# Performance work log

Hardware: AMD Instinct MI355X
Metric: run time of the kernel (lower is better)

The kernel has to match this reference:

```python
import jax, jax.numpy as jnp
import numpy as np

VERY_NEG = -1e11
VERY_SMALL = 1e-10
PAGERANK_LAMBDA = 0.8
FACT_SCALE = 3.0


def _linear(x, W, b):
    return x @ W.T + b


def _lstm(x, Wih, Whh, bih, bhh):
    # single-layer unidirectional LSTM, pytorch gate order (i, f, g, o)
    B, T, _ = x.shape
    H = Whh.shape[1]
    def step(carry, xt):
        h, c = carry
        g = xt @ Wih.T + bih + h @ Whh.T + bhh
        i, f, gg, o = jnp.split(g, 4, axis=-1)
        c = jax.nn.sigmoid(f) * c + jax.nn.sigmoid(i) * jnp.tanh(gg)
        h = jax.nn.sigmoid(o) * jnp.tanh(c)
        return (h, c), h
    init = (jnp.zeros((B, H), x.dtype), jnp.zeros((B, H), x.dtype))
    (h_last, _), hs = jax.lax.scan(step, init, jnp.swapaxes(x, 0, 1))
    return jnp.swapaxes(hs, 0, 1), h_last


def _forward(local_entity, q2e_adj_mat, kb_fact_rel, query_text, e2f_entity, f2e_entity,
             answer_dist, word_emb, entity_emb, rel_emb, ent_W, ent_b, rel_W, rel_b,
             lstm_Wih, lstm_Whh, lstm_bih, lstm_bhh, q2e_W, q2e_b, head_W, head_b,
             tail_W, tail_b, self_W, self_b, e2e_W, e2e_b, score_W, score_b):
    B, E = local_entity.shape
    D = ent_W.shape[0]
    num_word = word_emb.shape[0] - 1
    num_entity = entity_emb.shape[0] - 1
    b_idx = jnp.arange(B)[:, None]  # (B,1) for batched gather/scatter

    # --- query LSTM encoder ---
    query_mask = (query_text != num_word).astype(jnp.float32)            # (B,Q)
    qh, q_last = _lstm(word_emb[query_text], lstm_Wih, lstm_Whh, lstm_bih, lstm_bhh)
    query_node_emb = q_last[:, None, :]                                   # (B,1,D)

    # --- fact embeddings + fact-query attention weights ---
    local_fact_emb = _linear(rel_emb[kb_fact_rel], rel_W, rel_b)          # (B,F,D)
    div = jnp.sqrt(jnp.asarray(D, jnp.float32))
    sim = jnp.einsum('bqd,bfd->bqf', qh, local_fact_emb) / div
    sim = jax.nn.softmax(sim + (1.0 - query_mask)[:, :, None] * VERY_NEG, axis=1)
    att = jnp.einsum('bqf,bqd->bfd', sim, qh)                             # (B,F,D)
    Wf = jnp.sum(att * local_fact_emb, axis=2) / div                      # (B,F)
    W_tilde = jnp.exp(Wf - jnp.max(Wf, axis=1, keepdims=True))
    # e2f_softmax[b,e] = sum of W_tilde over facts whose head is e (sparse e2f^T @ W_tilde)
    e2f_softmax = jnp.maximum(
        jnp.zeros((B, E), jnp.float32).at[b_idx, e2f_entity].add(W_tilde), VERY_SMALL)

    # --- entity embeddings (word_dim != entity_dim -> entity_linear) ---
    local_entity_emb = _linear(entity_emb[local_entity], ent_W, ent_b)    # (B,E,D)
    pagerank_f = q2e_adj_mat[:, :, 0]                                     # (B,E)

    n_layer = q2e_W.shape[0]
    for i in range(n_layer):
        q2e_emb = jnp.broadcast_to(_linear(query_node_emb, q2e_W[i], q2e_b[i]), (B, E, D))
        # entity -> fact: gather head-entity messages
        head = _linear(local_entity_emb, head_W[i], head_b[i])            # (B,E,D)
        e2f_emb = jax.nn.relu(
            _linear(local_fact_emb, self_W[i], self_b[i]) + head[b_idx, e2f_entity])
        pr = pagerank_f / e2f_softmax                                     # (B,E)
        e2f_norm = (W_tilde * pr[b_idx, e2f_entity])[:, :, None]          # (B,F,1)
        e2f_emb = e2f_emb * e2f_norm
        # fact -> entity: scatter-add to tail entities
        tail = _linear(e2f_emb, tail_W[i], tail_b[i])                     # (B,F,D)
        f2e_emb = jax.nn.relu(
            _linear(local_entity_emb, self_W[i], self_b[i])
            + jnp.zeros((B, E, D), jnp.float32).at[b_idx, f2e_entity].add(tail))
        pagerank_f = (PAGERANK_LAMBDA
                      * jnp.zeros((B, E), jnp.float32).at[b_idx, f2e_entity].add(e2f_norm[:, :, 0])
                      + (1.0 - PAGERANK_LAMBDA) * pagerank_f)
        nxt = jnp.concatenate([local_entity_emb, q2e_emb, FACT_SCALE * f2e_emb], axis=2)
        local_entity_emb = jax.nn.relu(_linear(nxt, e2e_W[i], e2e_b[i]))

    score = local_entity_emb @ score_W + score_b                          # (B,E)
    mask = (local_entity != num_entity).astype(jnp.float32)
    score = score + (1.0 - mask) * VERY_NEG
    return jax.nn.sigmoid(score) * mask


def setup_inputs() -> dict:
    key = jax.random.key(0)
    ks = jax.random.split(key, 24)
    B, E, Fc, Q = 8, 2000, 12000, 20
    WD, D = 300, 100
    NE, NW, NR, L = 100000, 40000, 300, 3
    f32 = jnp.float32
    def nrm(k, shape, scale):
        return jax.random.normal(k, shape, f32) * scale
    return {
        'local_entity': jax.random.randint(ks[0], (B, E), 0, NE),
        'q2e_adj_mat': jax.random.uniform(ks[1], (B, E, 1), f32),
        'kb_fact_rel': jax.random.randint(ks[2], (B, Fc), 0, NR),
        'query_text': jax.random.randint(ks[3], (B, Q), 0, NW),
        'e2f_entity': jax.random.randint(ks[4], (B, Fc), 0, E),
        'f2e_entity': jax.random.randint(ks[5], (B, Fc), 0, E),
        'answer_dist': jax.random.uniform(ks[6], (B, E), f32),
        'word_emb': nrm(ks[7], (NW + 1, WD), 0.02),
        'entity_emb': nrm(ks[8], (NE + 1, WD), 0.02),
        'rel_emb': nrm(ks[9], (NR + 1, 2 * WD), 0.02),
        'ent_W': nrm(ks[10], (D, WD), WD ** -0.5), 'ent_b': jnp.zeros((D,), f32),
        'rel_W': nrm(ks[11], (D, 2 * WD), (2 * WD) ** -0.5), 'rel_b': jnp.zeros((D,), f32),
        'lstm_Wih': nrm(ks[12], (4 * D, WD), WD ** -0.5),
        'lstm_Whh': nrm(ks[13], (4 * D, D), D ** -0.5),
        'lstm_bih': jnp.zeros((4 * D,), f32), 'lstm_bhh': jnp.zeros((4 * D,), f32),
        'q2e_W': nrm(ks[14], (L, D, D), D ** -0.5), 'q2e_b': jnp.zeros((L, D), f32),
        'head_W': nrm(ks[15], (L, D, D), D ** -0.5), 'head_b': jnp.zeros((L, D), f32),
        'tail_W': nrm(ks[16], (L, D, D), D ** -0.5), 'tail_b': jnp.zeros((L, D), f32),
        'self_W': nrm(ks[17], (L, D, D), D ** -0.5), 'self_b': jnp.zeros((L, D), f32),
        'e2e_W': nrm(ks[18], (L, D, 3 * D), (3 * D) ** -0.5), 'e2e_b': jnp.zeros((L, D), f32),
        'score_W': nrm(ks[19], (D,), D ** -0.5), 'score_b': jnp.zeros((), f32),
    }


def reference(local_entity, q2e_adj_mat, kb_fact_rel, query_text, e2f_entity, f2e_entity,
              answer_dist, word_emb, entity_emb, rel_emb, ent_W, ent_b, rel_W, rel_b,
              lstm_Wih, lstm_Whh, lstm_bih, lstm_bhh, q2e_W, q2e_b, head_W, head_b,
              tail_W, tail_b, self_W, self_b, e2e_W, e2e_b, score_W, score_b):
    return _forward(local_entity, q2e_adj_mat, kb_fact_rel, query_text, e2f_entity,
                    f2e_entity, answer_dist, word_emb, entity_emb, rel_emb, ent_W, ent_b,
                    rel_W, rel_b, lstm_Wih, lstm_Whh, lstm_bih, lstm_bhh, q2e_W, q2e_b,
                    head_W, head_b, tail_W, tail_b, self_W, self_b, e2e_W, e2e_b,
                    score_W, score_b)
```

## Files before the change

kernel.cpp:

```cpp
#include <hip/hip_runtime.h>
#include <math.h>

#define VERY_NEG  -100000000000.0f
#define VERY_SMALLF 1e-10f

constexpr int B  = 8;
constexpr int E  = 2000;
constexpr int FC = 12000;
constexpr int Q  = 20;
constexpr int WD = 300;
constexpr int D  = 100;
constexpr int NW = 40000;
constexpr int NE = 100000;
constexpr int G4 = 4 * D;
constexpr int NREL = 301;
constexpr int NF = B * FC;
constexpr int NR_ = B * E;
constexpr int NRP = 16384;

__device__ __forceinline__ float sigmoidf_(float x) { return 1.0f / (1.0f + expf(-x)); }

__device__ __forceinline__ void tile16(const float* __restrict__ As_, const float* __restrict__ Bs_,
                                       int rg, int cgc, float acc[4][4]) {
#pragma unroll 5
    for (int k4 = 0; k4 < 25; ++k4) {
        float a_[4][4], b_[4][4];
#pragma unroll
        for (int i = 0; i < 4; ++i) {
            float4 v = *(const float4*)&As_[(rg * 4 + i) * 104 + k4 * 4];
            a_[i][0] = v.x; a_[i][1] = v.y; a_[i][2] = v.z; a_[i][3] = v.w;
        }
#pragma unroll
        for (int kk = 0; kk < 4; ++kk) {
            float4 v = *(const float4*)&Bs_[(k4 * 4 + kk) * 100 + cgc * 4];
            b_[kk][0] = v.x; b_[kk][1] = v.y; b_[kk][2] = v.z; b_[kk][3] = v.w;
        }
#pragma unroll
        for (int kk = 0; kk < 4; ++kk)
#pragma unroll
            for (int i = 0; i < 4; ++i)
#pragma unroll
                for (int j = 0; j < 4; ++j)
                    acc[i][j] += a_[i][kk] * b_[kk][j];
    }
}

__device__ __forceinline__ void stage_B100(const float* __restrict__ Wt, int ldW, int col0, int k0,
                                           float* __restrict__ Bs_) {
    for (int i = threadIdx.x; i < 2500; i += 256) {
        int k = i / 25, d2 = i - k * 25;
        *(float4*)&Bs_[k * 100 + d2 * 4] = *(const float4*)&Wt[(size_t)(k0 + k) * ldW + col0 + d2 * 4];
    }
}

__device__ void gemm_tile_g(const float* __restrict__ A, int K,
                            const int* __restrict__ rix, int nrows,
                            const float* __restrict__ Wt, int ldW, int col0,
                            const float* __restrict__ bias,
                            float* __restrict__ C,
                            int base, float* As_, float* Bs_) {
    int tid = threadIdx.x;
    int cg_ = tid & 31, rg = tid >> 5, cgc = cg_ < 25 ? cg_ : 24;
    float acc[4][4] = {{0.f}};
    for (int k0 = 0; k0 < K; k0 += 100) {
        __syncthreads();
        for (int i = tid; i < 800; i += 256) {
            int r = i / 25, c = i - r * 25;
            int rr = base + r; if (rr >= nrows) rr = nrows - 1;
            int gr = rix ? rix[rr] : rr;
            *(float4*)&As_[r * 104 + c * 4] = *(const float4*)&A[(size_t)gr * K + k0 + c * 4];
        }
        stage_B100(Wt, ldW, col0, k0, Bs_);
        __syncthreads();
        tile16(As_, Bs_, rg, cgc, acc);
    }
    if (cg_ < 25) {
        float4 bb = *(const float4*)&bias[col0 + cg_ * 4];
#pragma unroll
        for (int i = 0; i < 4; ++i) {
            int r = base + rg * 4 + i;
            if (r < nrows) {
                float4 o;
                o.x = acc[i][0] + bb.x; o.y = acc[i][1] + bb.y;
                o.z = acc[i][2] + bb.z; o.w = acc[i][3] + bb.w;
                *(float4*)&C[(size_t)r * ldW + col0 + cg_ * 4] = o;
            }
        }
    }
}

__device__ void gemm_tile_512(const float* __restrict__ A, int K,
                              const int* __restrict__ rix, int nrows,
                              const float* __restrict__ Wt, int ldW, int col0,
                              const float* __restrict__ bias,
                              float* __restrict__ C,
                              int base, float* As_, float* Bs_) {
    int tid = threadIdx.x;
    int cg_ = tid & 31, rg = (tid >> 5) & 7, cgc = cg_ < 25 ? cg_ : 24;
    bool on = tid < 256;
    float acc[4][4] = {{0.f}};
    for (int k0 = 0; k0 < K; k0 += 100) {
        __syncthreads();
        for (int i = tid; i < 800; i += 512) {
            int r = i / 25, c = i - r * 25;
            int rr = base + r; if (rr >= nrows) rr = nrows - 1;
            int gr = rix ? rix[rr] : rr;
            *(float4*)&As_[r * 104 + c * 4] = *(const float4*)&A[(size_t)gr * K + k0 + c * 4];
        }
        for (int i = tid; i < 2500; i += 512) {
            int k = i / 25, d2 = i - k * 25;
            *(float4*)&Bs_[k * 100 + d2 * 4] = *(const float4*)&Wt[(size_t)(k0 + k) * ldW + col0 + d2 * 4];
        }
        __syncthreads();
        if (on) tile16(As_, Bs_, rg, cgc, acc);
    }
    if (on && cg_ < 25) {
        float4 bb = *(const float4*)&bias[col0 + cg_ * 4];
#pragma unroll
        for (int i = 0; i < 4; ++i) {
            int r = base + rg * 4 + i;
            if (r < nrows) {
                float4 o;
                o.x = acc[i][0] + bb.x; o.y = acc[i][1] + bb.y;
                o.z = acc[i][2] + bb.z; o.w = acc[i][3] + bb.w;
                *(float4*)&C[(size_t)r * ldW + col0 + cg_ * 4] = o;
            }
        }
    }
}

struct PrepP {
    const float *ent_W, *rel_W, *Wih, *Whh, *head_W, *self_W, *tail_W, *e2e_W, *bih, *bhh, *q2e_adj;
    float *entWt, *relWt, *WihT, *WhhT, *headWt, *selfWt, *tailWt, *e2eWt, *bihh, *pr, *e2f_sm;
    int *cnt, *present;
};

__device__ void tr_tile(const float* __restrict__ in, float* __restrict__ out, int M, int K,
                        int kx, int my, float tb[32][33]) {
    int x = threadIdx.x & 31, y = threadIdx.x >> 5;
    int k0 = kx * 32, m0 = my * 32;
    for (int yy = y; yy < 32; yy += 8) {
        int m = m0 + yy, k = k0 + x;
        if (m < M && k < K) tb[yy][x] = in[(size_t)m * K + k];
    }
    __syncthreads();
    for (int yy = y; yy < 32; yy += 8) {
        int k = k0 + yy, m = m0 + x;
        if (m < M && k < K) out[(size_t)k * M + m] = tb[x][yy];
    }
}

__global__ __launch_bounds__(256) void k_prep(PrepP p) {
    __shared__ float tb[32][33];
    int j = blockIdx.x, tid = threadIdx.x;
    if (j < 40)       { tr_tile(p.ent_W, p.entWt, 100, 300, j % 10, j / 10, tb); }
    else if (j < 116) { j -= 40;  tr_tile(p.rel_W, p.relWt, 100, 600, j % 19, j / 19, tb); }
    else if (j < 246) { j -= 116; tr_tile(p.Wih, p.WihT, 400, 300, j % 10, j / 10, tb); }
    else if (j < 298) { j -= 246; tr_tile(p.Whh, p.WhhT, 400, 100, j % 4, j / 4, tb); }
    else if (j < 346) { j -= 298; int z = j / 16, t = j % 16; tr_tile(p.head_W + z * 10000, p.headWt + z * 10000, 100, 100, t % 4, t / 4, tb); }
    else if (j < 394) { j -= 346; int z = j / 16, t = j % 16; tr_tile(p.self_W + z * 10000, p.selfWt + z * 10000, 100, 100, t % 4, t / 4, tb); }
    else if (j < 442) { j -= 394; int z = j / 16, t = j % 16; tr_tile(p.tail_W + z * 10000, p.tailWt + z * 10000, 100, 100, t % 4, t / 4, tb); }
    else if (j < 562) { j -= 442; int z = j / 40, t = j % 40; tr_tile(p.e2e_W + z * 30000, p.e2eWt + z * 30000, 100, 300, t % 10, t / 10, tb); }
    else if (j < 564) { int idx = (j - 562) * 256 + tid; if (idx < G4) p.bihh[idx] = p.bih[idx] + p.bhh[idx]; }
    else if (j < 580) { int idx = (j - 564) * 256 + tid; if (idx < 4000) ((float4*)p.pr)[idx] = ((const float4*)p.q2e_adj)[idx]; }
    else if (j < 596) { int idx = (j - 580) * 256 + tid; if (idx < 4096) ((int4*)p.cnt)[idx] = make_int4(0, 0, 0, 0); }
    else if (j < 612) { int idx = (j - 596) * 256 + tid; if (idx < 4000) ((float4*)p.e2f_sm)[idx] = make_float4(0.f, 0.f, 0.f, 0.f); }
    else              { int idx = (j - 612) * 256 + tid; if (idx < B * NREL) p.present[idx] = 0; }
}

__global__ void k_hist(const int* __restrict__ f2e, const int* __restrict__ kb_rel,
                       int* __restrict__ cnt, int* __restrict__ present) {
    int fid = blockIdx.x * 256 + threadIdx.x;
    if (fid >= NF) return;
    int b = fid / FC;
    atomicAdd(&cnt[b * E + f2e[fid]], 1);
    present[b * NREL + kb_rel[fid]] = 1;
}

struct F1P {
    const int *cnt; int *off, *cursor; float *cnt_f;
    const float *word_emb; const int *qtext; const float *WihT, *bihh; float *xW;
    const float *rel_emb, *relWt, *rel_b; float *rel_proj;
};

__device__ void scan_block(const int* __restrict__ cnt, int* __restrict__ off,
                           int* __restrict__ cursor, float* __restrict__ cnt_f, int* part) {
    int t = threadIdx.x;
    int s = 0;
    const int4* c4 = (const int4*)(cnt + t * 64);
#pragma unroll 4
    for (int i = 0; i < 16; ++i) { int4 v = c4[i]; s += v.x + v.y + v.z + v.w; }
    part[t] = s;
    __syncthreads();
    for (int d = 1; d < 256; d <<= 1) {
        int add = (t >= d) ? part[t - d] : 0;
        __syncthreads();
        part[t] += add;
        __syncthreads();
    }
    int run = part[t] - s;
    for (int i = 0; i < 64; ++i) {
        int idx = t * 64 + i;
        if (idx < NR_) {
            off[idx] = run; cursor[idx] = run; cnt_f[idx] = (float)cnt[idx];
            run += cnt[idx];
        }
    }
    if (t == 255) off[NR_] = part[255];
}

__global__ __launch_bounds__(256) void k_front1(F1P p) {
    __shared__ float smem[13328];
    int j = blockIdx.x;
    if (j == 0) {
        scan_block(p.cnt, p.off, p.cursor, p.cnt_f, (int*)smem);
    } else if (j <= 20) {
        j -= 1;
        gemm_tile_g(p.word_emb, WD, p.qtext, B * Q, p.WihT, G4, (j / 5) * 100, p.bihh,
                    p.xW, (j % 5) * 32, smem, smem + 3328);
    } else {
        j -= 21;
        gemm_tile_g(p.rel_emb, 2 * WD, nullptr, NREL, p.relWt, D, 0, p.rel_b,
                    p.rel_proj, j * 32, smem, smem + 3328);
    }
}

struct F2P {
    const float *xW, *WhhT, *q2e_W, *q2e_b; float *qh, *q2e_vec;
    const float *rel_proj, *selfWt, *self_b; float *self_proj;
};

__device__ void lstm_block(int b, const F2P& p, float* smem) {
    float* h = smem; float* c = smem + 128; float* gate = smem + 256;
    int t = threadIdx.x;
    float w[100];
    if (t < G4) {
#pragma unroll
        for (int j = 0; j < 100; ++j) w[j] = p.WhhT[j * G4 + t];
    }
    if (t < D) { h[t] = 0.f; c[t] = 0.f; }
    __syncthreads();
    for (int step = 0; step < Q; ++step) {
        if (t < G4) {
            float a0 = 0.f, a1 = 0.f, a2 = 0.f, a3 = 0.f;
#pragma unroll
            for (int k4 = 0; k4 < 25; ++k4) {
                float4 hv = *(const float4*)&h[k4 * 4];
                a0 += hv.x * w[k4 * 4 + 0];
                a1 += hv.y * w[k4 * 4 + 1];
                a2 += hv.z * w[k4 * 4 + 2];
                a3 += hv.w * w[k4 * 4 + 3];
            }
            gate[t] = p.xW[(b * Q + step) * G4 + t] + ((a0 + a1) + (a2 + a3));
        }
        __syncthreads();
        if (t < D) {
            float ig = sigmoidf_(gate[t]);
            float fg = sigmoidf_(gate[D + t]);
            float gg = tanhf(gate[2 * D + t]);
            float og = sigmoidf_(gate[3 * D + t]);
            float cn = fg * c[t] + ig * gg;
            c[t] = cn;
            float hn = og * tanhf(cn);
            h[t] = hn;
            p.qh[(b * Q + step) * D + t] = hn;
        }
        __syncthreads();
    }
    if (t < 3 * D) {
        int l = t / D, d = t - l * D;
        float acc = p.q2e_b[l * D + d];
        const float* W = p.q2e_W + (size_t)(l * D + d) * D;
        for (int k = 0; k < D; ++k) acc += h[k] * W[k];
        p.q2e_vec[(l * B + b) * D + d] = acc;
    }
}

__global__ __launch_bounds__(512) void k_front2(F2P p) {
    __shared__ float smem[13328];
    int j = blockIdx.x;
    if (j < 8) {
        lstm_block(j, p, smem);
    } else {
        j -= 8;
        int z = j / 10, t = j % 10;
        gemm_tile_512(p.rel_proj, D, nullptr, NREL, p.selfWt + z * 10000, D, 0, p.self_b + z * 100,
                      p.self_proj + (size_t)z * NREL * D, t * 32, smem, smem + 3328);
    }
}

__global__ void k_wfall(const int* __restrict__ qtext, const float* __restrict__ qh,
                        const float* __restrict__ rel_proj, const int* __restrict__ present,
                        float* __restrict__ Wt_rel) {
    __shared__ float qh_s[Q * D];
    __shared__ float msk[Q];
    __shared__ float red[512];
    int b = blockIdx.x, t = threadIdx.x;
    for (int k = t; k < Q * D; k += 320) qh_s[k] = qh[b * Q * D + k];
    if (t < Q) msk[t] = (qtext[b * Q + t] != NW) ? 1.f : 0.f;
    if (t < 192) red[320 + t] = -INFINITY;
    __syncthreads();
    float wf = 0.f;
    bool active = t < NREL;
    if (active) {
        const float* lfe = rel_proj + t * D;
        float s[Q];
#pragma unroll
        for (int q = 0; q < Q; ++q) s[q] = 0.f;
        for (int k = 0; k < D; ++k) {
            float lv = lfe[k];
#pragma unroll
            for (int q = 0; q < Q; ++q) s[q] += qh_s[q * D + k] * lv;
        }
        float m = -INFINITY;
        float sv[Q];
#pragma unroll
        for (int q = 0; q < Q; ++q) {
            s[q] *= 0.1f;
            sv[q] = s[q] + (1.f - msk[q]) * VERY_NEG;
            m = fmaxf(m, sv[q]);
        }
        float sum = 0.f;
        float ex[Q];
#pragma unroll
        for (int q = 0; q < Q; ++q) { ex[q] = expf(sv[q] - m); sum += ex[q]; }
#pragma unroll
        for (int q = 0; q < Q; ++q) wf += (ex[q] / sum) * s[q];
    }
    red[t] = (active && present[b * NREL + t]) ? wf : -INFINITY;
    __syncthreads();
    for (int st = 256; st > 0; st >>= 1) {
        if (t < st) red[t] = fmaxf(red[t], red[t + st]);
        __syncthreads();
    }
    float m = red[0];
    if (active) Wt_rel[b * NREL + t] = expf(wf - m);
}

struct MidP {
    const int *f2e, *e2f, *kb_rel; const float *Wt_rel;
    int *cursor, *sorted; float *W_tilde, *e2f_sm;
    const float *entity_emb; const int *local_entity;
    const float *entWt, *ent_b, *headWt0, *head_b0, *selfWt0, *self_b0;
    float *lee, *head, *lee_self;
};

__device__ void lee_dual_tile32(int base, const MidP& p, float* As_, float* Bs_) {
    int tid = threadIdx.x;
    int cg_ = tid & 31, rg = tid >> 5, cgc = cg_ < 25 ? cg_ : 24;
    float acc[4][4] = {{0.f}};
    for (int k0 = 0; k0 < 300; k0 += 100) {
        __syncthreads();
        for (int i = tid; i < 800; i += 256) {
            int r = i / 25, c = i - r * 25;
            int gr = p.local_entity[base + r];
            *(float4*)&As_[r * 104 + c * 4] = *(const float4*)&p.entity_emb[(size_t)gr * 300 + k0 + c * 4];
        }
        stage_B100(p.entWt, 100, 0, k0, Bs_);
        __syncthreads();
        tile16(As_, Bs_, rg, cgc, acc);
    }
    __syncthreads();
    if (cg_ < 25) {
        float4 bb = *(const float4*)&p.ent_b[cg_ * 4];
#pragma unroll
        for (int i = 0; i < 4; ++i) {
            int r = base + rg * 4 + i;
            float4 o;
            o.x = acc[i][0] + bb.x; o.y = acc[i][1] + bb.y;
            o.z = acc[i][2] + bb.z; o.w = acc[i][3] + bb.w;
            *(float4*)&p.lee[(size_t)r * 100 + cg_ * 4] = o;
            *(float4*)&As_[(rg * 4 + i) * 104 + cg_ * 4] = o;
        }
    }
    stage_B100(p.headWt0, 100, 0, 0, Bs_);
    __syncthreads();
    float acc2[4][4] = {{0.f}};
    tile16(As_, Bs_, rg, cgc, acc2);
    if (cg_ < 25) {
        float4 bb = *(const float4*)&p.head_b0[cg_ * 4];
#pragma unroll
        for (int i = 0; i < 4; ++i) {
            int r = base + rg * 4 + i;
            float4 o;
            o.x = acc2[i][0] + bb.x; o.y = acc2[i][1] + bb.y;
            o.z = acc2[i][2] + bb.z; o.w = acc2[i][3] + bb.w;
            *(float4*)&p.head[(size_t)r * 100 + cg_ * 4] = o;
        }
    }
    __syncthreads();
    stage_B100(p.selfWt0, 100, 0, 0, Bs_);
    __syncthreads();
    float acc3[4][4] = {{0.f}};
    tile16(As_, Bs_, rg, cgc, acc3);
    if (cg_ < 25) {
        float4 bb = *(const float4*)&p.self_b0[cg_ * 4];
#pragma unroll
        for (int i = 0; i < 4; ++i) {
            int r = base + rg * 4 + i;
            float4 o;
            o.x = acc3[i][0] + bb.x; o.y = acc3[i][1] + bb.y;
            o.z = acc3[i][2] + bb.z; o.w = acc3[i][3] + bb.w;
            *(float4*)&p.lee_self[(size_t)r * 100 + cg_ * 4] = o;
        }
    }
}

__global__ __launch_bounds__(256) void k_mid(MidP p) {
    __shared__ float smem[13328];
    int j = blockIdx.x, tid = threadIdx.x;
    if (j < 500) {
        lee_dual_tile32(j * 32, p, smem, smem + 3328);
    } else {
        int fid = (j - 500) * 256 + tid;
        int b = fid / FC;
        int pos = atomicAdd(&p.cursor[b * E + p.f2e[fid]], 1);
        p.sorted[pos] = fid;
        float wt = p.Wt_rel[b * NREL + p.kb_rel[fid]];
        p.W_tilde[fid] = wt;
        atomicAdd(&p.e2f_sm[b * E + p.e2f[fid]], wt);
    }
}

__global__ void k_gfact(const int* __restrict__ sorted, const int* __restrict__ kb_rel,
                        const int* __restrict__ e2f, const float* __restrict__ W_tilde,
                        const float* __restrict__ e2f_sm,
                        int* __restrict__ es_rel_s, float* __restrict__ g_s) {
    int j = blockIdx.x * 256 + threadIdx.x;
    if (j >= NF) return;
    int fid = sorted[j];
    int b = fid / FC;
    int es = e2f[fid], rel = kb_rel[fid];
    es_rel_s[j] = es | (rel << 16);
    g_s[j] = W_tilde[fid] / fmaxf(e2f_sm[b * E + es], VERY_SMALLF);
}

__global__ __launch_bounds__(256) void k_gather(const int* __restrict__ es_rel_s,
                                                const float* __restrict__ g_s,
                                                const int* __restrict__ off,
                                                const float* __restrict__ self_proj_l,
                                                const float* __restrict__ head,
                                                const float* __restrict__ pr,
                                                float* __restrict__ u, float* __restrict__ pr_acc) {
    int bid = blockIdx.x;
    int job = (bid & 7) * 500 + (bid >> 3);
    int wave = threadIdx.x >> 6, lane = threadIdx.x & 63;
    int ri = job * 4 + wave;
    int b = ri / E, bE = b * E;
    int s = off[ri], e = off[ri + 1];
    float a0 = 0.f, a1 = 0.f, ns = 0.f;
    const float* hb = head + (size_t)bE * D;
    const float* prb = pr + bE;
    for (int cs = s; cs < e; cs += 64) {
        int cnt = e - cs; if (cnt > 64) cnt = 64;
        int erl = 0; float njl = 0.f;
        if (lane < cnt) {
            erl = es_rel_s[cs + lane];
            njl = g_s[cs + lane] * prb[erl & 0xffff];
        }
        for (int j = 0; j < cnt; ++j) {
            int er = __shfl(erl, j);
            float nj = __shfl(njl, j);
            int es = er & 0xffff, rel = er >> 16;
            const float* sp = self_proj_l + rel * D;
            const float* hr = hb + (size_t)es * D;
            a0 += nj * fmaxf(0.f, sp[lane] + hr[lane]);
            if (lane < 36) a1 += nj * fmaxf(0.f, sp[lane + 64] + hr[lane + 64]);
            ns += nj;
        }
    }
    u[(size_t)ri * D + lane] = a0;
    if (lane < 36) u[(size_t)ri * D + 64 + lane] = a1;
    if (lane == 0) pr_acc[ri] = ns;
}

struct TailP {
    const float *u, *cnt_f, *tailWt_l, *tail_b_l;
    const float *cur, *lee_self_in, *q2e_l, *e2eWt_l, *e2e_b_l;
    const float *pr_acc_c; float *pr; float *nxt;
    const float *headWt_n, *head_b_n, *selfWt_n, *self_b_n;
    float *head, *lee_self_out;
    int last; const int *local_entity; const float *score_W, *score_b; float *out;
};

__global__ __launch_bounds__(256) void k_tailent(TailP p) {
    __shared__ float As_[32 * 104];
    __shared__ float Bs_[100 * 100];
    __shared__ float Fs_[32 * 104];
    int tid = threadIdx.x, base = blockIdx.x * 32;
    int cg_ = tid & 31, rg = tid >> 5, cgc = cg_ < 25 ? cg_ : 24;
    for (int i = tid; i < 800; i += 256) {
        int r = i / 25, c = i - r * 25;
        *(float4*)&As_[r * 104 + c * 4] = *(const float4*)&p.u[(size_t)(base + r) * 100 + c * 4];
    }
    stage_B100(p.tailWt_l, 100, 0, 0, Bs_);
    __syncthreads();
    float accF[4][4] = {{0.f}};
    tile16(As_, Bs_, rg, cgc, accF);
    __syncthreads();
    if (cg_ < 25) {
        float4 tbv = *(const float4*)&p.tail_b_l[cg_ * 4];
#pragma unroll
        for (int i = 0; i < 4; ++i) {
            int r = base + rg * 4 + i;
            float cf = p.cnt_f[r];
            float4 ls = *(const float4*)&p.lee_self_in[(size_t)r * 100 + cg_ * 4];
            float4 o;
            o.x = 3.f * fmaxf(0.f, ls.x + accF[i][0] + cf * tbv.x);
            o.y = 3.f * fmaxf(0.f, ls.y + accF[i][1] + cf * tbv.y);
            o.z = 3.f * fmaxf(0.f, ls.z + accF[i][2] + cf * tbv.z);
            o.w = 3.f * fmaxf(0.f, ls.w + accF[i][3] + cf * tbv.w);
            *(float4*)&Fs_[(rg * 4 + i) * 104 + cg_ * 4] = o;
        }
    }
    if (tid < 32) {
        int r = base + tid;
        p.pr[r] = 0.8f * p.pr_acc_c[r] + 0.2f * p.pr[r];
    }
    float acc[4][4] = {{0.f}};
    __syncthreads();
    for (int i = tid; i < 800; i += 256) {
        int r = i / 25, c = i - r * 25;
        *(float4*)&As_[r * 104 + c * 4] = *(const float4*)&p.cur[(size_t)(base + r) * 100 + c * 4];
    }
    stage_B100(p.e2eWt_l, 100, 0, 0, Bs_);
    __syncthreads();
    tile16(As_, Bs_, rg, cgc, acc);
    __syncthreads();
    for (int i = tid; i < 800; i += 256) {
        int r = i / 25, c = i - r * 25;
        int bb = (base + r) / E;
        *(float4*)&As_[r * 104 + c * 4] = *(const float4*)&p.q2e_l[bb * 100 + c * 4];
    }
    stage_B100(p.e2eWt_l, 100, 0, 100, Bs_);
    __syncthreads();
    tile16(As_, Bs_, rg, cgc, acc);
    __syncthreads();
    stage_B100(p.e2eWt_l, 100, 0, 200, Bs_);
    __syncthreads();
    tile16(Fs_, Bs_, rg, cgc, acc);
    __syncthreads();
    if (cg_ < 25) {
        float4 ebv = *(const float4*)&p.e2e_b_l[cg_ * 4];
#pragma unroll
        for (int i = 0; i < 4; ++i) {
            int r = base + rg * 4 + i;
            float4 o;
            o.x = fmaxf(acc[i][0] + ebv.x, 0.f); o.y = fmaxf(acc[i][1] + ebv.y, 0.f);
            o.z = fmaxf(acc[i][2] + ebv.z, 0.f); o.w = fmaxf(acc[i][3] + ebv.w, 0.f);
            *(float4*)&p.nxt[(size_t)r * 100 + cg_ * 4] = o;
            *(float4*)&As_[(rg * 4 + i) * 104 + cg_ * 4] = o;
        }
    }
    if (!p.last) {
        stage_B100(p.headWt_n, 100, 0, 0, Bs_);
        __syncthreads();
        float a2[4][4] = {{0.f}};
        tile16(As_, Bs_, rg, cgc, a2);
        if (cg_ < 25) {
            float4 bb = *(const float4*)&p.head_b_n[cg_ * 4];
#pragma unroll
            for (int i = 0; i < 4; ++i) {
                int r = base + rg * 4 + i;
                float4 o;
                o.x = a2[i][0] + bb.x; o.y = a2[i][1] + bb.y;
                o.z = a2[i][2] + bb.z; o.w = a2[i][3] + bb.w;
                *(float4*)&p.head[(size_t)r * 100 + cg_ * 4] = o;
            }
        }
        __syncthreads();
        stage_B100(p.selfWt_n, 100, 0, 0, Bs_);
        __syncthreads();
        float a3[4][4] = {{0.f}};
        tile16(As_, Bs_, rg, cgc, a3);
        if (cg_ < 25) {
            float4 bb = *(const float4*)&p.self_b_n[cg_ * 4];
#pragma unroll
            for (int i = 0; i < 4; ++i) {
                int r = base + rg * 4 + i;
                float4 o;
                o.x = a3[i][0] + bb.x; o.y = a3[i][1] + bb.y;
                o.z = a3[i][2] + bb.z; o.w = a3[i][3] + bb.w;
                *(float4*)&p.lee_self_out[(size_t)r * 100 + cg_ * 4] = o;
            }
        }
    } else {
        __syncthreads();
        if (tid < 32) {
            int r = base + tid;
            if (p.local_entity[r] == NE) { p.out[r] = 0.f; }
            else {
                float a = p.score_b[0];
                for (int k = 0; k < D; ++k) a += As_[tid * 104 + k] * p.score_W[k];
                p.out[r] = 1.f / (1.f + expf(-a));
            }
        }
    }
}

extern "C" void kernel_launch(void* const* d_in, const int* in_sizes, int n_in,
                              void* d_out, int out_size, void* d_ws, size_t ws_size,
                              hipStream_t stream) {
    const int*   local_entity = (const int*)d_in[0];
    const float* q2e_adj      = (const float*)d_in[1];
    const int*   kb_rel       = (const int*)d_in[2];
    const int*   qtext        = (const int*)d_in[3];
    const int*   e2f          = (const int*)d_in[4];
    const int*   f2e          = (const int*)d_in[5];
    const float* word_emb     = (const float*)d_in[7];
    const float* entity_emb   = (const float*)d_in[8];
    const float* rel_emb      = (const float*)d_in[9];
    const float* ent_W        = (const float*)d_in[10];
    const float* ent_b        = (const float*)d_in[11];
    const float* rel_W        = (const float*)d_in[12];
    const float* rel_b        = (const float*)d_in[13];
    const float* lstm_Wih     = (const float*)d_in[14];
    const float* lstm_Whh     = (const float*)d_in[15];
    const float* lstm_bih     = (const float*)d_in[16];
    const float* lstm_bhh     = (const float*)d_in[17];
    const float* q2e_W        = (const float*)d_in[18];
    const float* q2e_b        = (const float*)d_in[19];
    const float* head_W       = (const float*)d_in[20];
    const float* head_b       = (const float*)d_in[21];
    const float* tail_W       = (const float*)d_in[22];
    const float* tail_b       = (const float*)d_in[23];
    const float* self_W       = (const float*)d_in[24];
    const float* self_b       = (const float*)d_in[25];
    const float* e2e_W        = (const float*)d_in[26];
    const float* e2e_b        = (const float*)d_in[27];
    const float* score_W      = (const float*)d_in[28];
    const float* score_b      = (const float*)d_in[29];

    float* ws = (float*)d_ws;
    float* rel_proj  = ws;
    float* self_proj = rel_proj  + NREL * D;
    float* xW        = self_proj + 3 * NREL * D;
    float* qh        = xW        + B * Q * G4;
    float* q2e_vec   = qh        + B * Q * D;
    float* Wt_rel    = q2e_vec   + 3 * B * D;
    float* W_tilde   = Wt_rel    + B * NREL;
    float* e2f_sm    = W_tilde   + NF;
    float* leeA      = e2f_sm    + NR_;
    float* leeB      = leeA      + NR_ * D;
    float* head      = leeB      + NR_ * D;
    float* lee_self  = head      + NR_ * D;
    float* u_buf     = lee_self  + NR_ * D;
    float* pr        = u_buf     + NR_ * D;
    float* pr_acc    = pr        + NR_;
    float* cnt_f     = pr_acc    + NR_;
    float* g_s       = cnt_f     + NR_;
    float* entWt     = g_s       + NF;
    float* relWt     = entWt     + WD * D;
    float* WihT      = relWt     + 2 * WD * D;
    float* WhhT      = WihT      + WD * G4;
    float* headWt    = WhhT      + D * G4;
    float* selfWt    = headWt    + 3 * D * D;
    float* tailWt    = selfWt    + 3 * D * D;
    float* e2eWt     = tailWt    + 3 * D * D;
    float* bihh      = e2eWt     + 9 * D * D;
    int*   present   = (int*)(bihh + G4);
    int*   cnt       = present   + B * NREL;
    int*   cursor    = cnt       + NRP;
    int*   off       = cursor    + NR_;
    int*   sorted    = off       + NR_ + 1;
    int*   es_rel_s  = sorted    + NF;

    PrepP pp;
    pp.ent_W = ent_W; pp.rel_W = rel_W; pp.Wih = lstm_Wih; pp.Whh = lstm_Whh;
    pp.head_W = head_W; pp.self_W = self_W; pp.tail_W = tail_W; pp.e2e_W = e2e_W;
    pp.bih = lstm_bih; pp.bhh = lstm_bhh; pp.q2e_adj = q2e_adj;
    pp.entWt = entWt; pp.relWt = relWt; pp.WihT = WihT; pp.WhhT = WhhT;
    pp.headWt = headWt; pp.selfWt = selfWt; pp.tailWt = tailWt; pp.e2eWt = e2eWt;
    pp.bihh = bihh; pp.pr = pr; pp.e2f_sm = e2f_sm; pp.cnt = cnt; pp.present = present;
    k_prep<<<615, 256, 0, stream>>>(pp);

    k_hist<<<375, 256, 0, stream>>>(f2e, kb_rel, cnt, present);

    F1P f1;
    f1.cnt = cnt; f1.off = off; f1.cursor = cursor; f1.cnt_f = cnt_f;
    f1.word_emb = word_emb; f1.qtext = qtext; f1.WihT = WihT; f1.bihh = bihh; f1.xW = xW;
    f1.rel_emb = rel_emb; f1.relWt = relWt; f1.rel_b = rel_b; f1.rel_proj = rel_proj;
    k_front1<<<31, 256, 0, stream>>>(f1);

    F2P f2;
    f2.xW = xW; f2.WhhT = WhhT; f2.q2e_W = q2e_W; f2.q2e_b = q2e_b;
    f2.qh = qh; f2.q2e_vec = q2e_vec;
    f2.rel_proj = rel_proj; f2.selfWt = selfWt; f2.self_b = self_b; f2.self_proj = self_proj;
    k_front2<<<38, 512, 0, stream>>>(f2);

    k_wfall<<<B, 320, 0, stream>>>(qtext, qh, rel_proj, present, Wt_rel);

    MidP mp;
    mp.f2e = f2e; mp.e2f = e2f; mp.kb_rel = kb_rel; mp.Wt_rel = Wt_rel;
    mp.cursor = cursor; mp.sorted = sorted; mp.W_tilde = W_tilde; mp.e2f_sm = e2f_sm;
    mp.entity_emb = entity_emb; mp.local_entity = local_entity;
    mp.entWt = entWt; mp.ent_b = ent_b;
    mp.headWt0 = headWt; mp.head_b0 = head_b; mp.selfWt0 = selfWt; mp.self_b0 = self_b;
    mp.lee = leeA; mp.head = head; mp.lee_self = lee_self;
    k_mid<<<500 + 375, 256, 0, stream>>>(mp);

    k_gfact<<<375, 256, 0, stream>>>(sorted, kb_rel, e2f, W_tilde, e2f_sm, es_rel_s, g_s);

    float* cur = leeA; float* nxt = leeB;
    for (int l = 0; l < 3; ++l) {
        k_gather<<<4000, 256, 0, stream>>>(es_rel_s, g_s, off, self_proj + (size_t)l * NREL * D,
                                           head, pr, u_buf, pr_acc);
        TailP tp;
        tp.u = u_buf; tp.cnt_f = cnt_f;
        tp.tailWt_l = tailWt + l * 10000; tp.tail_b_l = tail_b + l * 100;
        tp.cur = cur; tp.lee_self_in = lee_self; tp.q2e_l = q2e_vec + l * B * D;
        tp.e2eWt_l = e2eWt + l * 30000; tp.e2e_b_l = e2e_b + l * 100;
        tp.pr_acc_c = pr_acc; tp.pr = pr; tp.nxt = nxt;
        int ln = (l < 2) ? l + 1 : l;
        tp.headWt_n = headWt + ln * 10000; tp.head_b_n = head_b + ln * 100;
        tp.selfWt_n = selfWt + ln * 10000; tp.self_b_n = self_b + ln * 100;
        tp.head = head; tp.lee_self_out = lee_self;
        tp.last = (l == 2); tp.local_entity = local_entity;
        tp.score_W = score_W; tp.score_b = score_b; tp.out = (float*)d_out;
        k_tailent<<<NR_ / 32, 256, 0, stream>>>(tp);
        float* t = cur; cur = nxt; nxt = t;
    }
}
```

Before: 348.2 us.

## Fuse per-layer gather and tail-entity update into one kernel with ping-pong buffers

Merges the gather kernel (weighted fact aggregation per entity) into the tail/entity update kernel, so each block first aggregates its 32 rows into shared memory and then runs the dense matmuls on them. This removes the u/pr_acc global round-trip and one launch per layer. Since blocks now read head/lee_self/pr while others write them, those buffers are double-buffered across layers. Each block handles 8 gather rows per wave serially, giving 500 blocks instead of 4000, which may reduce latency hiding for the irregular gather.

```diff
diff --git a/kernel.cpp b/kernel.cpp
--- a/kernel.cpp
+++ b/kernel.cpp
@@ -435,68 +435,67 @@
     g_s[j] = W_tilde[fid] / fmaxf(e2f_sm[b * E + es], VERY_SMALLF);
 }
 
-__global__ __launch_bounds__(256) void k_gather(const int* __restrict__ es_rel_s,
-                                                const float* __restrict__ g_s,
-                                                const int* __restrict__ off,
-                                                const float* __restrict__ self_proj_l,
-                                                const float* __restrict__ head,
-                                                const float* __restrict__ pr,
-                                                float* __restrict__ u, float* __restrict__ pr_acc) {
-    int bid = blockIdx.x;
-    int job = (bid & 7) * 500 + (bid >> 3);
-    int wave = threadIdx.x >> 6, lane = threadIdx.x & 63;
-    int ri = job * 4 + wave;
-    int b = ri / E, bE = b * E;
-    int s = off[ri], e = off[ri + 1];
-    float a0 = 0.f, a1 = 0.f, ns = 0.f;
-    const float* hb = head + (size_t)bE * D;
-    const float* prb = pr + bE;
-    for (int cs = s; cs < e; cs += 64) {
-        int cnt = e - cs; if (cnt > 64) cnt = 64;
-        int erl = 0; float njl = 0.f;
-        if (lane < cnt) {
-            erl = es_rel_s[cs + lane];
-            njl = g_s[cs + lane] * prb[erl & 0xffff];
-        }
-        for (int j = 0; j < cnt; ++j) {
-            int er = __shfl(erl, j);
-            float nj = __shfl(njl, j);
-            int es = er & 0xffff, rel = er >> 16;
-            const float* sp = self_proj_l + rel * D;
-            const float* hr = hb + (size_t)es * D;
-            a0 += nj * fmaxf(0.f, sp[lane] + hr[lane]);
-            if (lane < 36) a1 += nj * fmaxf(0.f, sp[lane + 64] + hr[lane + 64]);
-            ns += nj;
-        }
-    }
-    u[(size_t)ri * D + lane] = a0;
-    if (lane < 36) u[(size_t)ri * D + 64 + lane] = a1;
-    if (lane == 0) pr_acc[ri] = ns;
-}
-
-struct TailP {
-    const float *u, *cnt_f, *tailWt_l, *tail_b_l;
+struct LayerP {
+    const int *es_rel_s; const float *g_s; const int *off;
+    const float *self_proj_l;
+    const float *head_in, *pr_in;
+    float *pr_out;
+    const float *cnt_f;
+    const float *tailWt_l, *tail_b_l;
     const float *cur, *lee_self_in, *q2e_l, *e2eWt_l, *e2e_b_l;
-    const float *pr_acc_c; float *pr; float *nxt;
+    float *nxt;
     const float *headWt_n, *head_b_n, *selfWt_n, *self_b_n;
-    float *head, *lee_self_out;
+    float *head_out, *lee_self_out;
     int last; const int *local_entity; const float *score_W, *score_b; float *out;
 };
 
-__global__ __launch_bounds__(256) void k_tailent(TailP p) {
+__global__ __launch_bounds__(256) void k_layer(LayerP p) {
+    __shared__ float Us_[32 * 104];
+    __shared__ float Bs_[100 * 100];
     __shared__ float As_[32 * 104];
-    __shared__ float Bs_[100 * 100];
-    __shared__ float Fs_[32 * 104];
-    int tid = threadIdx.x, base = blockIdx.x * 32;
+    __shared__ float pa_[32];
+    int bid = blockIdx.x;
+    int xcd = bid & 7, idx = bid >> 3;
+    int job = (xcd < 4 ? xcd * 63 : 4 * 63 + (xcd - 4) * 62) + idx;
+    int base = job * 32;
+    int tid = threadIdx.x;
+    int wave = tid >> 6, lane = tid & 63;
+    for (int rr = 0; rr < 8; ++rr) {
+        int lr = wave * 8 + rr;
+        int ri = base + lr;
+        int b = ri / E, bE = b * E;
+        int s = p.off[ri], e = p.off[ri + 1];
+        float a0 = 0.f, a1 = 0.f, ns = 0.f;
+        const float* hb = p.head_in + (size_t)bE * D;
+        const float* prb = p.pr_in + bE;
+        for (int cs = s; cs < e; cs += 64) {
+            int cnt = e - cs; if (cnt > 64) cnt = 64;
+            int erl = 0; float njl = 0.f;
+            if (lane < cnt) {
+                erl = p.es_rel_s[cs + lane];
+                njl = p.g_s[cs + lane] * prb[erl & 0xffff];
+            }
+            for (int j = 0; j < cnt; ++j) {
+                int er = __shfl(erl, j);
+                float nj = __shfl(njl, j);
+                int es = er & 0xffff, rel = er >> 16;
+                const float* sp = p.self_proj_l + rel * D;
+                const float* hr = hb + (size_t)es * D;
+                a0 += nj * fmaxf(0.f, sp[lane] + hr[lane]);
+                if (lane < 36) a1 += nj * fmaxf(0.f, sp[lane + 64] + hr[lane + 64]);
+                ns += nj;
+            }
+        }
+        Us_[lr * 104 + lane] = a0;
+        if (lane < 36) Us_[lr * 104 + 64 + lane] = a1;
+        if (lane == 0) pa_[lr] = ns;
+    }
+    __syncthreads();
+    stage_B100(p.tailWt_l, 100, 0, 0, Bs_);
+    __syncthreads();
     int cg_ = tid & 31, rg = tid >> 5, cgc = cg_ < 25 ? cg_ : 24;
-    for (int i = tid; i < 800; i += 256) {
-        int r = i / 25, c = i - r * 25;
-        *(float4*)&As_[r * 104 + c * 4] = *(const float4*)&p.u[(size_t)(base + r) * 100 + c * 4];
-    }
-    stage_B100(p.tailWt_l, 100, 0, 0, Bs_);
-    __syncthreads();
     float accF[4][4] = {{0.f}};
-    tile16(As_, Bs_, rg, cgc, accF);
+    tile16(Us_, Bs_, rg, cgc, accF);
     __syncthreads();
     if (cg_ < 25) {
         float4 tbv = *(const float4*)&p.tail_b_l[cg_ * 4];
@@ -510,12 +509,12 @@
             o.y = 3.f * fmaxf(0.f, ls.y + accF[i][1] + cf * tbv.y);
             o.z = 3.f * fmaxf(0.f, ls.z + accF[i][2] + cf * tbv.z);
             o.w = 3.f * fmaxf(0.f, ls.w + accF[i][3] + cf * tbv.w);
-            *(float4*)&Fs_[(rg * 4 + i) * 104 + cg_ * 4] = o;
+            *(float4*)&Us_[(rg * 4 + i) * 104 + cg_ * 4] = o;
         }
     }
     if (tid < 32) {
         int r = base + tid;
-        p.pr[r] = 0.8f * p.pr_acc_c[r] + 0.2f * p.pr[r];
+        p.pr_out[r] = 0.8f * pa_[tid] + 0.2f * p.pr_in[r];
     }
     float acc[4][4] = {{0.f}};
     __syncthreads();
@@ -538,7 +537,7 @@
     __syncthreads();
     stage_B100(p.e2eWt_l, 100, 0, 200, Bs_);
     __syncthreads();
-    tile16(Fs_, Bs_, rg, cgc, acc);
+    tile16(Us_, Bs_, rg, cgc, acc);
     __syncthreads();
     if (cg_ < 25) {
         float4 ebv = *(const float4*)&p.e2e_b_l[cg_ * 4];
@@ -565,7 +564,7 @@
                 float4 o;
                 o.x = a2[i][0] + bb.x; o.y = a2[i][1] + bb.y;
                 o.z = a2[i][2] + bb.z; o.w = a2[i][3] + bb.w;
-                *(float4*)&p.head[(size_t)r * 100 + cg_ * 4] = o;
+                *(float4*)&p.head_out[(size_t)r * 100 + cg_ * 4] = o;
             }
         }
         __syncthreads();
@@ -585,7 +584,6 @@
             }
         }
     } else {
-        __syncthreads();
         if (tid < 32) {
             int r = base + tid;
             if (p.local_entity[r] == NE) { p.out[r] = 0.f; }
@@ -642,12 +640,13 @@
     float* e2f_sm    = W_tilde   + NF;
     float* leeA      = e2f_sm    + NR_;
     float* leeB      = leeA      + NR_ * D;
-    float* head      = leeB      + NR_ * D;
-    float* lee_self  = head      + NR_ * D;
-    float* u_buf     = lee_self  + NR_ * D;
-    float* pr        = u_buf     + NR_ * D;
-    float* pr_acc    = pr        + NR_;
-    float* cnt_f     = pr_acc    + NR_;
+    float* headA     = leeB      + NR_ * D;
+    float* headB     = headA     + NR_ * D;
+    float* lee_selfA = headB     + NR_ * D;
+    float* lee_selfB = lee_selfA + NR_ * D;
+    float* prA       = lee_selfB + NR_ * D;
+    float* prB       = prA       + NR_;
+    float* cnt_f     = prB       + NR_;
     float* g_s       = cnt_f     + NR_;
     float* entWt     = g_s       + NF;
     float* relWt     = entWt     + WD * D;
@@ -671,7 +670,7 @@
     pp.bih = lstm_bih; pp.bhh = lstm_bhh; pp.q2e_adj = q2e_adj;
     pp.entWt = entWt; pp.relWt = relWt; pp.WihT = WihT; pp.WhhT = WhhT;
     pp.headWt = headWt; pp.selfWt = selfWt; pp.tailWt = tailWt; pp.e2eWt = e2eWt;
-    pp.bihh = bihh; pp.pr = pr; pp.e2f_sm = e2f_sm; pp.cnt = cnt; pp.present = present;
+    pp.bihh = bihh; pp.pr = prA; pp.e2f_sm = e2f_sm; pp.cnt = cnt; pp.present = present;
     k_prep<<<615, 256, 0, stream>>>(pp);
 
     k_hist<<<375, 256, 0, stream>>>(f2e, kb_rel, cnt, present);
@@ -696,28 +695,35 @@
     mp.entity_emb = entity_emb; mp.local_entity = local_entity;
     mp.entWt = entWt; mp.ent_b = ent_b;
     mp.headWt0 = headWt; mp.head_b0 = head_b; mp.selfWt0 = selfWt; mp.self_b0 = self_b;
-    mp.lee = leeA; mp.head = head; mp.lee_self = lee_self;
+    mp.lee = leeA; mp.head = headA; mp.lee_self = lee_selfA;
     k_mid<<<500 + 375, 256, 0, stream>>>(mp);
 
     k_gfact<<<375, 256, 0, stream>>>(sorted, kb_rel, e2f, W_tilde, e2f_sm, es_rel_s, g_s);
 
-    float* cur = leeA; float* nxt = leeB;
+    float* curL[3]  = {leeA, leeB, leeA};
+    float* nxtL[3]  = {leeB, leeA, leeB};
+    float* hIn[3]   = {headA, headB, headA};
+    float* hOut[3]  = {headB, headA, headB};
+    float* lsIn[3]  = {lee_selfA, lee_selfB, lee_selfA};
+    float* lsOut[3] = {lee_selfB, lee_selfA, lee_selfB};
+    float* pIn[3]   = {prA, prB, prA};
+    float* pOut[3]  = {prB, prA, prB};
     for (int l = 0; l < 3; ++l) {
-        k_gather<<<4000, 256, 0, stream>>>(es_rel_s, g_s, off, self_proj + (size_t)l * NREL * D,
-                                           head, pr, u_buf, pr_acc);
-        TailP tp;
-        tp.u = u_buf; tp.cnt_f = cnt_f;
-        tp.tailWt_l = tailWt + l * 10000; tp.tail_b_l = tail_b + l * 100;
-        tp.cur = cur; tp.lee_self_in = lee_self; tp.q2e_l = q2e_vec + l * B * D;
-        tp.e2eWt_l = e2eWt + l * 30000; tp.e2e_b_l = e2e_b + l * 100;
-        tp.pr_acc_c = pr_acc; tp.pr = pr; tp.nxt = nxt;
+        LayerP lp;
+        lp.es_rel_s = es_rel_s; lp.g_s = g_s; lp.off = off;
+        lp.self_proj_l = self_proj + (size_t)l * NREL * D;
+        lp.head_in = hIn[l]; lp.pr_in = pIn[l]; lp.pr_out = pOut[l];
+        lp.cnt_f = cnt_f;
+        lp.tailWt_l = tailWt + l * 10000; lp.tail_b_l = tail_b + l * 100;
+        lp.cur = curL[l]; lp.lee_self_in = lsIn[l]; lp.q2e_l = q2e_vec + l * B * D;
+        lp.e2eWt_l = e2eWt + l * 30000; lp.e2e_b_l = e2e_b + l * 100;
+        lp.nxt = nxtL[l];
         int ln = (l < 2) ? l + 1 : l;
-        tp.headWt_n = headWt + ln * 10000; tp.head_b_n = head_b + ln * 100;
-        tp.selfWt_n = selfWt + ln * 10000; tp.self_b_n = self_b + ln * 100;
-        tp.head = head; tp.lee_self_out = lee_self;
-        tp.last = (l == 2); tp.local_entity = local_entity;
-        tp.score_W = score_W; tp.score_b = score_b; tp.out = (float*)d_out;
-        k_tailent<<<NR_ / 32, 256, 0, stream>>>(tp);
-        float* t = cur; cur = nxt; nxt = t;
-    }
-}
+        lp.headWt_n = headWt + ln * 10000; lp.head_b_n = head_b + ln * 100;
+        lp.selfWt_n = selfWt + ln * 10000; lp.self_b_n = self_b + ln * 100;
+        lp.head_out = hOut[l]; lp.lee_self_out = lsOut[l];
+        lp.last = (l == 2); lp.local_entity = local_entity;
+        lp.score_W = score_W; lp.score_b = score_b; lp.out = (float*)d_out;
+        k_layer<<<500, 256, 0, stream>>>(lp);
+    }
+}
```

Result: slower. 371.9 us (+6.8%).
